# Performance work log

Hardware: AMD Instinct MI355X
Metric: run time of the kernel (lower is better)

Reference implementation:

```python
import jax, jax.numpy as jnp
import numpy as np

HIDDEN = 512
HEADS = 8
HEAD_DIM = HIDDEN // HEADS


def setup_inputs() -> dict:
    key = jax.random.key(0)
    ks = jax.random.split(key, 13)
    B, S, H = 4, 2048, HIDDEN
    s = 1.0 / np.sqrt(H).astype(np.float32)
    inp = {
        "values": jax.random.normal(ks[0], (B, S, H), jnp.float32),
        "keys": jax.random.normal(ks[1], (B, S, H), jnp.float32),
        "query": jax.random.normal(ks[2], (B, S, H), jnp.float32),
        "mask": jax.random.randint(ks[3], (B, S), 0, 2, jnp.int32),
        "Wq": jax.random.normal(ks[4], (H, H), jnp.float32) * s,
        "bq": jnp.zeros((H,), jnp.float32),
        "Wk": jax.random.normal(ks[5], (H, H), jnp.float32) * s,
        "bk": jnp.zeros((H,), jnp.float32),
        "Wv": jax.random.normal(ks[6], (H, H), jnp.float32) * s,
        "bv": jnp.zeros((H,), jnp.float32),
        "Wo": jax.random.normal(ks[7], (H, H), jnp.float32) * s,
        "bo": jnp.zeros((H,), jnp.float32),
    }
    return inp


def reference(values, keys, query, mask, Wq, bq, Wk, bk, Wv, bv, Wo, bo):
    B, Sq, H = query.shape
    Sk = keys.shape[1]
    # projections (x @ W + b)
    Q = query @ Wq + bq
    K = keys @ Wk + bk
    V = values @ Wv + bv
    # [B, S, H] -> [B, heads, S, head_dim]
    def split(x, S):
        return x.reshape(B, S, HEADS, HEAD_DIM).transpose(0, 2, 1, 3)
    Qh, Kh, Vh = split(Q, Sq), split(K, Sk), split(V, Sk)
    scale = 1.0 / np.sqrt(HEAD_DIM).astype(np.float32)
    scores = jnp.einsum('bhqd,bhkd->bhqk', Qh, Kh) * scale  # [B,H,Sq,Sk]
    m = mask[:, None, None, :]  # [B,1,1,Sk]
    scores = jnp.where(m == 0, jnp.float32(-1e9), scores)
    attn = jax.nn.softmax(scores, axis=-1)
    ctx = jnp.einsum('bhqk,bhkd->bhqd', attn, Vh)
    ctx = ctx.transpose(0, 2, 1, 3).reshape(B, Sq, H)
    return ctx @ Wo + bo
```

## Files before the change

kernel.cpp:

```cpp
#include <hip/hip_runtime.h>

#define HID 512
#define NH 8
#define HD 64
#define BATCH 4
#define SEQ 2048
#define MTOT (BATCH * SEQ)

typedef unsigned short ushort_t;
typedef __bf16 bf16x8 __attribute__((ext_vector_type(8)));
typedef unsigned short ushort8v __attribute__((ext_vector_type(8)));
typedef unsigned short ushort4v __attribute__((ext_vector_type(4)));
typedef float floatx4 __attribute__((ext_vector_type(4)));
typedef unsigned int uintx4 __attribute__((ext_vector_type(4)));

static __device__ __forceinline__ unsigned short f2bf(float f) {
  __bf16 b = (__bf16)f;
  return __builtin_bit_cast(unsigned short, b);
}
static __device__ __forceinline__ float bf2f(unsigned short s) {
  union { unsigned int u; float f; } c; c.u = ((unsigned int)s) << 16;
  return c.f;
}
static __device__ __forceinline__ bf16x8 asbf(ushort8v v) {
  return __builtin_bit_cast(bf16x8, v);
}
static __device__ __forceinline__ float max3f(float a, float b, float c) {
  return fmaxf(fmaxf(a, b), c);
}
static __device__ __forceinline__ float fexp2(float x) {
  return __builtin_amdgcn_exp2f(x);
}
static __device__ __forceinline__ void gl_lds16(const ushort_t* g, ushort_t* l) {
  __builtin_amdgcn_global_load_lds(
      (const __attribute__((address_space(1))) void*)g,
      (__attribute__((address_space(3))) void*)l, 16, 0, 0);
}

#define SC_LOG2E 0.18033688011112042f

__global__ void detect_dtype(const unsigned int* __restrict__ q, int* __restrict__ flag) {
  if (threadIdx.x == 0 && blockIdx.x == 0) {
    int hits = 0;
    for (int i = 0; i < 256; ++i) {
      unsigned e = (q[i] >> 7) & 0xff;
      hits += (e >= 110 && e <= 136) ? 1 : 0;
    }
    flag[0] = (hits >= 128) ? 1 : 0;
  }
}

__global__ __launch_bounds__(256) void prep_w(
    const void* __restrict__ W0, const void* __restrict__ W1,
    const void* __restrict__ W2, const void* __restrict__ W3,
    ushort_t* __restrict__ T0, ushort_t* __restrict__ T1,
    ushort_t* __restrict__ T2, ushort_t* __restrict__ T3,
    const int* __restrict__ flag) {
  const int isbf = flag[0];
  const void* W; ushort_t* T;
  switch (blockIdx.y) {
    case 0: W = W0; T = T0; break;
    case 1: W = W1; T = T1; break;
    case 2: W = W2; T = T2; break;
    default: W = W3; T = T3; break;
  }
  __shared__ ushort_t Ts[64 * 72];
  const int tid = threadIdx.x;
  const int kt = (blockIdx.x >> 3) * 64;
  const int nt = (blockIdx.x & 7) * 64;
  const int r = tid >> 2;
  const int c = (tid & 3) * 16;

  ushort8v v0, v1;
  if (isbf) {
    const ushort_t* p = (const ushort_t*)W + (long)(kt + r) * HID + nt + c;
    v0 = *(const ushort8v*)(p);
    v1 = *(const ushort8v*)(p + 8);
  } else {
    const float* p = (const float*)W + (long)(kt + r) * HID + nt + c;
    floatx4 f0 = *(const floatx4*)(p);
    floatx4 f1 = *(const floatx4*)(p + 4);
    floatx4 f2 = *(const floatx4*)(p + 8);
    floatx4 f3 = *(const floatx4*)(p + 12);
#pragma unroll
    for (int i = 0; i < 4; ++i) {
      v0[i] = f2bf(f0[i]); v0[4 + i] = f2bf(f1[i]);
      v1[i] = f2bf(f2[i]); v1[4 + i] = f2bf(f3[i]);
    }
  }
  *(ushort8v*)(&Ts[r * 72 + c])     = v0;
  *(ushort8v*)(&Ts[r * 72 + c + 8]) = v1;
  __syncthreads();
  ushort8v o0, o1;
#pragma unroll
  for (int j = 0; j < 8; ++j) o0[j] = Ts[(c + j) * 72 + r];
#pragma unroll
  for (int j = 0; j < 8; ++j) o1[j] = Ts[(c + 8 + j) * 72 + r];
  ushort_t* q = T + (long)(nt + r) * HID + kt + c;
  *(ushort8v*)(q)     = o0;
  *(ushort8v*)(q + 8) = o1;
}

__global__ __launch_bounds__(256) void prep_b(
    const void* __restrict__ B0, const void* __restrict__ B1,
    const void* __restrict__ B2, const void* __restrict__ B3,
    float* __restrict__ biasF, const int* __restrict__ flag) {
  const int isbf = flag[0];
  int i = blockIdx.x * 256 + threadIdx.x;
  int t = i >> 9, j = i & 511;
  const void* B = (t == 0) ? B0 : (t == 1) ? B1 : (t == 2) ? B2 : B3;
  biasF[i] = isbf ? bf2f(((const ushort_t*)B)[j]) : ((const float*)B)[j];
}

__global__ __launch_bounds__(256) void prep_mask(
    const int* __restrict__ mask, float* __restrict__ mb) {
  int i = blockIdx.x * 256 + threadIdx.x;
  mb[i] = mask[i] ? 0.f : -1e9f;
}

__global__ __launch_bounds__(256) void gemm_qkv3(
    const void* __restrict__ X0, const void* __restrict__ X1, const void* __restrict__ X2,
    const ushort_t* __restrict__ WtBase, const float* __restrict__ biasBase,
    ushort_t* __restrict__ YBase, const int* __restrict__ flag) {
  const int isbf = flag[0];
  int lin = blockIdx.x + 256 * blockIdx.z;
  int swz = (lin & 7) * 96 + (lin >> 3);
  const int z = swz >> 8;
  const int mblk = swz & 255;
  const void* X = (z == 0) ? X0 : (z == 1) ? X1 : X2;
  const ushort_t* Wt = WtBase + (size_t)z * HID * HID;
  const float* biasF = biasBase + (size_t)z * HID;
  ushort_t* Y = YBase + (size_t)z * MTOT * HID;

  const int tid = threadIdx.x;
  const int wid = tid >> 6, lane = tid & 63;
  const int id = lane & 15, quad = lane >> 4;
  const int m0 = mblk * 32;

  __shared__ ushort_t As[32 * 32];
  __shared__ ushort_t Bs[512 * 32];

  const int a_r = tid >> 3;
  const int a_b = (tid & 7) >> 1;
  const int a_o = (tid & 1) * 4;
  const int a_pb = a_b ^ (a_r & 3);
  const int b_ro = lane >> 2;
  const int b_scb = (lane & 3);

  floatx4 acc[2][8];
#pragma unroll
  for (int i = 0; i < 2; ++i)
#pragma unroll
    for (int j = 0; j < 8; ++j) acc[i][j] = (floatx4){0.f, 0.f, 0.f, 0.f};

  for (int k0 = 0; k0 < HID; k0 += 32) {
    ushort4v aW;
    if (isbf) {
      aW = *(const ushort4v*)((const ushort_t*)X + (long)(m0 + a_r) * HID + k0 + (tid & 7) * 4);
    } else {
      floatx4 f = *(const floatx4*)((const float*)X + (long)(m0 + a_r) * HID + k0 + (tid & 7) * 4);
#pragma unroll
      for (int i = 0; i < 4; ++i) aW[i] = f2bf(f[i]);
    }
    __syncthreads();
    *(ushort4v*)(&As[a_r * 32 + (a_pb << 3) + a_o]) = aW;
#pragma unroll
    for (int i = 0; i < 8; ++i) {
      int rb = wid * 128 + i * 16;
      int srow = rb + b_ro;
      gl_lds16(Wt + (long)srow * HID + k0 + ((b_scb ^ (srow & 3)) << 3), &Bs[rb * 32]);
    }
    __syncthreads();
    {
      ushort8v af[2], bfv[8];
      const int pb = (quad ^ (id & 3)) << 3;
#pragma unroll
      for (int ms = 0; ms < 2; ++ms)
        af[ms] = *(const ushort8v*)(&As[(ms * 16 + id) * 32 + pb]);
#pragma unroll
      for (int ns = 0; ns < 8; ++ns)
        bfv[ns] = *(const ushort8v*)(&Bs[(wid * 128 + ns * 16 + id) * 32 + pb]);
#pragma unroll
      for (int ms = 0; ms < 2; ++ms)
#pragma unroll
        for (int ns = 0; ns < 8; ++ns)
          acc[ms][ns] = __builtin_amdgcn_mfma_f32_16x16x32_bf16(asbf(af[ms]), asbf(bfv[ns]), acc[ms][ns], 0, 0, 0);
    }
  }
#pragma unroll
  for (int ns = 0; ns < 8; ++ns) {
    int col = wid * 128 + ns * 16 + id;
    float bv = biasF[col];
#pragma unroll
    for (int ms = 0; ms < 2; ++ms) {
      int row0 = m0 + ms * 16 + quad * 4;
#pragma unroll
      for (int r = 0; r < 4; ++r)
        Y[(long)(row0 + r) * HID + col] = f2bf(acc[ms][ns][r] + bv);
    }
  }
}

__global__ __launch_bounds__(256) void gemm_out2(
    const ushort_t* __restrict__ X, const ushort_t* __restrict__ Wt,
    const float* __restrict__ biasF, void* __restrict__ out,
    const int* __restrict__ flag) {
  const int isbf = flag[0];
  const int tid = threadIdx.x;
  const int wid = tid >> 6, lane = tid & 63;
  const int id = lane & 15, quad = lane >> 4;
  const int wm = wid >> 1, wn = wid & 1;
  const int m0 = blockIdx.x * 64, n0 = blockIdx.y * 128;

  __shared__ ushort_t As[64 * 64];
  __shared__ ushort_t Bs[128 * 64];

  const int lrow = lane >> 3;
  const int scb  = (lane & 7) ^ lrow;

  floatx4 acc[2][4];
#pragma unroll
  for (int i = 0; i < 2; ++i)
#pragma unroll
    for (int j = 0; j < 4; ++j) acc[i][j] = (floatx4){0.f, 0.f, 0.f, 0.f};

  for (int k0 = 0; k0 < HID; k0 += 64) {
    __syncthreads();
#pragma unroll
    for (int i = 0; i < 2; ++i) {
      int r = wid * 16 + i * 8 + lrow;
      gl_lds16(X + (long)(m0 + r) * HID + k0 + scb * 8, &As[(wid * 16 + i * 8) * 64]);
    }
#pragma unroll
    for (int i = 0; i < 4; ++i) {
      int r = wid * 32 + i * 8 + lrow;
      gl_lds16(Wt + (long)(n0 + r) * HID + k0 + scb * 8, &Bs[(wid * 32 + i * 8) * 64]);
    }
    __syncthreads();
#pragma unroll
    for (int kk = 0; kk < 64; kk += 32) {
      ushort8v af[2], bfv[4];
      const int cb = (kk >> 3) + quad;
#pragma unroll
      for (int ms = 0; ms < 2; ++ms) {
        int row = wm * 32 + ms * 16 + id;
        af[ms] = *(const ushort8v*)(&As[row * 64 + ((cb ^ (id & 7)) << 3)]);
      }
#pragma unroll
      for (int ns = 0; ns < 4; ++ns) {
        int row = wn * 64 + ns * 16 + id;
        bfv[ns] = *(const ushort8v*)(&Bs[row * 64 + ((cb ^ (id & 7)) << 3)]);
      }
#pragma unroll
      for (int ms = 0; ms < 2; ++ms)
#pragma unroll
        for (int ns = 0; ns < 4; ++ns)
          acc[ms][ns] = __builtin_amdgcn_mfma_f32_16x16x32_bf16(asbf(af[ms]), asbf(bfv[ns]), acc[ms][ns], 0, 0, 0);
    }
  }
#pragma unroll
  for (int ns = 0; ns < 4; ++ns) {
    int col = n0 + wn * 64 + ns * 16 + id;
    float bv = biasF[col];
#pragma unroll
    for (int ms = 0; ms < 2; ++ms) {
      int row0 = m0 + wm * 32 + ms * 16 + quad * 4;
      if (isbf) {
        ushort_t* o = (ushort_t*)out;
#pragma unroll
        for (int r = 0; r < 4; ++r) o[(long)(row0 + r) * HID + col] = f2bf(acc[ms][ns][r] + bv);
      } else {
        float* o = (float*)out;
#pragma unroll
        for (int r = 0; r < 4; ++r) o[(long)(row0 + r) * HID + col] = acc[ms][ns][r] + bv;
      }
    }
  }
}

__global__ __launch_bounds__(512) void flash_attn(
    const ushort_t* __restrict__ Q, const ushort_t* __restrict__ K,
    const ushort_t* __restrict__ V, const float* __restrict__ mb,
    ushort_t* __restrict__ ctx) {
  int lin = blockIdx.x + 16 * blockIdx.y + 128 * blockIdx.z;
  int swz = (lin & 7) * 64 + (lin >> 3);
  const int qblk = swz & 15, h = (swz >> 4) & 7, b = swz >> 7;
  const int tid = threadIdx.x;
  const int wid = tid >> 6, lane = tid & 63;
  const int id = lane & 15, quad = lane >> 4;

  __shared__ ushort_t Kt[64 * 72];
  __shared__ ushort_t Vt[64 * 72];
  __shared__ ushort_t Pl[8][16 * 72];

  const ushort_t* Qb = Q + (long)(b * SEQ + qblk * 128 + wid * 16) * HID + h * HD;
  const ushort_t* Kb = K + (long)(b * SEQ) * HID + h * HD;
  const ushort_t* Vb = V + (long)(b * SEQ) * HID + h * HD;
  const float* mrow = mb + b * SEQ;

  ushort8v qf[2];
#pragma unroll
  for (int kh = 0; kh < 2; ++kh)
    qf[kh] = *(const ushort8v*)(Qb + id * HID + kh * 32 + quad * 8);

  floatx4 o[4];
  float m_i = -1e30f, l_i = 0.f;
#pragma unroll
  for (int dg = 0; dg < 4; ++dg) o[dg] = (floatx4){0, 0, 0, 0};

  const bool kstager = (tid < 256);
  const int t2 = tid & 255;
  const int skey = t2 >> 2;
  const int sdc  = (t2 & 3) * 16;
  const int vkp  = (t2 & 31) * 2;
  const int vdc  = (t2 >> 5) * 8;

  ushort8v r0, r1;
  if (kstager) {
    const ushort_t* kpp = Kb + (long)skey * HID + sdc;
    r0 = *(const ushort8v*)(kpp);
    r1 = *(const ushort8v*)(kpp + 8);
  } else {
    const ushort_t* vp0 = Vb + (long)vkp * HID + vdc;
    r0 = *(const ushort8v*)(vp0);
    r1 = *(const ushort8v*)(vp0 + HID);
  }

  for (int kb = 0; kb < SEQ / 64; ++kb) {
    if (kstager) {
      *(ushort8v*)(&Kt[skey * 72 + sdc])     = r0;
      *(ushort8v*)(&Kt[skey * 72 + sdc + 8]) = r1;
    } else {
      uintx4 a = __builtin_bit_cast(uintx4, r0);
      uintx4 bq = __builtin_bit_cast(uintx4, r1);
#pragma unroll
      for (int j = 0; j < 4; ++j) {
        unsigned int d0 = __builtin_amdgcn_perm(bq[j], a[j], 0x05040100u);
        unsigned int d1 = __builtin_amdgcn_perm(bq[j], a[j], 0x07060302u);
        *(unsigned int*)(&Vt[(vdc + 2 * j) * 72 + vkp])     = d0;
        *(unsigned int*)(&Vt[(vdc + 2 * j + 1) * 72 + vkp]) = d1;
      }
    }
    __syncthreads();

    if (kb + 1 < SEQ / 64) {
      if (kstager) {
        const ushort_t* kpp = Kb + (long)((kb + 1) * 64 + skey) * HID + sdc;
        r0 = *(const ushort8v*)(kpp);
        r1 = *(const ushort8v*)(kpp + 8);
      } else {
        const ushort_t* vp0 = Vb + (long)((kb + 1) * 64 + vkp) * HID + vdc;
        r0 = *(const ushort8v*)(vp0);
        r1 = *(const ushort8v*)(vp0 + HID);
      }
    }

    floatx4 st[4];
    __builtin_amdgcn_s_setprio(1);
#pragma unroll
    for (int ks = 0; ks < 4; ++ks) {
      ushort8v kf0 = *(const ushort8v*)(&Kt[(ks * 16 + id) * 72 + quad * 8]);
      ushort8v kf1 = *(const ushort8v*)(&Kt[(ks * 16 + id) * 72 + 32 + quad * 8]);
      floatx4 a = (floatx4){0, 0, 0, 0};
      a = __builtin_amdgcn_mfma_f32_16x16x32_bf16(asbf(kf0), asbf(qf[0]), a, 0, 0, 0);
      a = __builtin_amdgcn_mfma_f32_16x16x32_bf16(asbf(kf1), asbf(qf[1]), a, 0, 0, 0);
      st[ks] = a;
    }
    __builtin_amdgcn_s_setprio(0);
#pragma unroll
    for (int ks = 0; ks < 4; ++ks) {
      floatx4 mbv = *(const floatx4*)(mrow + kb * 64 + ks * 16 + quad * 4);
#pragma unroll
      for (int r = 0; r < 4; ++r)
        st[ks][r] = fmaf(st[ks][r], SC_LOG2E, mbv[r]);
    }
    {
      float t0 = max3f(st[0][0], st[0][1], st[0][2]);
      float t1 = max3f(st[0][3], st[1][0], st[1][1]);
      float t2m = max3f(st[1][2], st[1][3], st[2][0]);
      float t3 = max3f(st[2][1], st[2][2], st[2][3]);
      float t4 = max3f(st[3][0], st[3][1], st[3][2]);
      float mx = max3f(t0, t1, st[3][3]);
      float mz = max3f(t2m, t3, t4);
      mx = fmaxf(mx, mz);
      mx = fmaxf(mx, __shfl_xor(mx, 16));
      mx = fmaxf(mx, __shfl_xor(mx, 32));
      if (!__all(mx - m_i <= 8.f)) {
        float mnew = fmaxf(m_i, mx);
        float alpha = fexp2(m_i - mnew);
        m_i = mnew;
        l_i *= alpha;
#pragma unroll
        for (int dg = 0; dg < 4; ++dg) o[dg] *= alpha;
      }
      float mcur = m_i;
      floatx4 rsv = (floatx4){0.f, 0.f, 0.f, 0.f};
#pragma unroll
      for (int ks = 0; ks < 4; ++ks) {
        ushort4v pk;
#pragma unroll
        for (int r = 0; r < 4; ++r) {
          float p = fexp2(st[ks][r] - mcur);
          rsv[r] += p;
          pk[r] = f2bf(p);
        }
        *(ushort4v*)(&Pl[wid][id * 72 + ks * 16 + quad * 4]) = pk;
      }
      float rs = (rsv[0] + rsv[1]) + (rsv[2] + rsv[3]);
      rs += __shfl_xor(rs, 16);
      rs += __shfl_xor(rs, 32);
      l_i += rs;
    }

    __builtin_amdgcn_s_setprio(1);
#pragma unroll
    for (int kc = 0; kc < 2; ++kc) {
      ushort8v pf = *(const ushort8v*)(&Pl[wid][id * 72 + kc * 32 + quad * 8]);
#pragma unroll
      for (int dg = 0; dg < 4; ++dg) {
        ushort8v vf = *(const ushort8v*)(&Vt[(dg * 16 + id) * 72 + kc * 32 + quad * 8]);
        o[dg] = __builtin_amdgcn_mfma_f32_16x16x32_bf16(asbf(vf), asbf(pf), o[dg], 0, 0, 0);
      }
    }
    __builtin_amdgcn_s_setprio(0);
    __syncthreads();
  }

  {
    float inv = 1.0f / l_i;
    long qrow = (long)(b * SEQ + qblk * 128 + wid * 16 + id);
#pragma unroll
    for (int dg = 0; dg < 4; ++dg) {
      ushort4v pk;
#pragma unroll
      for (int r = 0; r < 4; ++r) pk[r] = f2bf(o[dg][r] * inv);
      *(ushort4v*)(&ctx[qrow * HID + h * HD + dg * 16 + quad * 4]) = pk;
    }
  }
}

extern "C" void kernel_launch(void* const* d_in, const int* in_sizes, int n_in,
                              void* d_out, int out_size, void* d_ws, size_t ws_size,
                              hipStream_t stream) {
  const void* values = d_in[0];
  const void* keys   = d_in[1];
  const void* query  = d_in[2];
  const int*  mask   = (const int*)d_in[3];
  const void* Wq = d_in[4];  const void* bq = d_in[5];
  const void* Wk = d_in[6];  const void* bk = d_in[7];
  const void* Wv = d_in[8];  const void* bv = d_in[9];
  const void* Wo = d_in[10]; const void* bo = d_in[11];

  ushort_t* ws = (ushort_t*)d_ws;
  const size_t NEL = (size_t)MTOT * HID;
  ushort_t* Qp  = ws;
  ushort_t* Kp  = ws + NEL;
  ushort_t* Vp  = ws + 2 * NEL;
  ushort_t* Cp  = ws + 3 * NEL;
  ushort_t* WqT = ws + 4 * NEL;
  ushort_t* WkT = WqT + (size_t)HID * HID;
  ushort_t* WvT = WkT + (size_t)HID * HID;
  ushort_t* WoT = WvT + (size_t)HID * HID;
  float* biasF  = (float*)(WoT + (size_t)HID * HID);
  float* mbias  = biasF + 4 * HID;
  int* flag     = (int*)(mbias + (size_t)BATCH * SEQ);

  detect_dtype<<<1, 64, 0, stream>>>((const unsigned int*)query, flag);
  prep_w<<<dim3(64, 4), 256, 0, stream>>>(Wq, Wk, Wv, Wo, WqT, WkT, WvT, WoT, flag);
  prep_b<<<8, 256, 0, stream>>>(bq, bk, bv, bo, biasF, flag);
  prep_mask<<<MTOT / 256, 256, 0, stream>>>(mask, mbias);

  gemm_qkv3<<<dim3(MTOT / 32, 1, 3), 256, 0, stream>>>(
      query, keys, values, WqT, biasF, Qp, flag);

  flash_attn<<<dim3(SEQ / 128, NH, BATCH), 512, 0, stream>>>(Qp, Kp, Vp, mbias, Cp);

  gemm_out2<<<dim3(MTOT / 64, HID / 128), 256, 0, stream>>>(
      Cp, WoT, biasF + 3 * HID, d_out, flag);
}
```

Measured before the change: 235.7 us.

## Load K fragments directly to registers and double-buffer V tile in flash attention

The flash attention kernel now reads K fragments straight from global memory into registers, prefetching the next tile during softmax, instead of staging K through shared memory. V is double-buffered in shared memory, with global loads issued two tiles ahead, so the transpose-store for the next tile overlaps with compute on the current one. The dtype detection kernel is parallelised across a wavefront, and the bias and mask prep kernels are merged into one launch. This trades higher register pressure and uncoalesced per-lane K loads for fewer LDS round trips and less stalling on staging.

```diff
diff --git a/kernel.cpp b/kernel.cpp
--- a/kernel.cpp
+++ b/kernel.cpp
@@ -40,14 +40,16 @@
 #define SC_LOG2E 0.18033688011112042f
 
 __global__ void detect_dtype(const unsigned int* __restrict__ q, int* __restrict__ flag) {
-  if (threadIdx.x == 0 && blockIdx.x == 0) {
-    int hits = 0;
-    for (int i = 0; i < 256; ++i) {
-      unsigned e = (q[i] >> 7) & 0xff;
-      hits += (e >= 110 && e <= 136) ? 1 : 0;
-    }
-    flag[0] = (hits >= 128) ? 1 : 0;
-  }
+  int lane = threadIdx.x;
+  int hits = 0;
+#pragma unroll
+  for (int i = 0; i < 4; ++i) {
+    unsigned e = (q[lane * 4 + i] >> 7) & 0xff;
+    hits += (e >= 110 && e <= 136) ? 1 : 0;
+  }
+#pragma unroll
+  for (int s = 1; s < 64; s <<= 1) hits += __shfl_xor(hits, s);
+  if (lane == 0) flag[0] = (hits >= 128) ? 1 : 0;
 }
 
 __global__ __launch_bounds__(256) void prep_w(
@@ -101,21 +103,22 @@
   *(ushort8v*)(q + 8) = o1;
 }
 
-__global__ __launch_bounds__(256) void prep_b(
+__global__ __launch_bounds__(256) void prep_bm(
     const void* __restrict__ B0, const void* __restrict__ B1,
     const void* __restrict__ B2, const void* __restrict__ B3,
-    float* __restrict__ biasF, const int* __restrict__ flag) {
-  const int isbf = flag[0];
-  int i = blockIdx.x * 256 + threadIdx.x;
-  int t = i >> 9, j = i & 511;
-  const void* B = (t == 0) ? B0 : (t == 1) ? B1 : (t == 2) ? B2 : B3;
-  biasF[i] = isbf ? bf2f(((const ushort_t*)B)[j]) : ((const float*)B)[j];
-}
-
-__global__ __launch_bounds__(256) void prep_mask(
-    const int* __restrict__ mask, float* __restrict__ mb) {
-  int i = blockIdx.x * 256 + threadIdx.x;
-  mb[i] = mask[i] ? 0.f : -1e9f;
+    float* __restrict__ biasF, const int* __restrict__ mask,
+    float* __restrict__ mb, const int* __restrict__ flag) {
+  const int blk = blockIdx.x;
+  if (blk < 8) {
+    const int isbf = flag[0];
+    int i = blk * 256 + threadIdx.x;
+    int t = i >> 9, j = i & 511;
+    const void* B = (t == 0) ? B0 : (t == 1) ? B1 : (t == 2) ? B2 : B3;
+    biasF[i] = isbf ? bf2f(((const ushort_t*)B)[j]) : ((const float*)B)[j];
+  } else {
+    int i = (blk - 8) * 256 + threadIdx.x;
+    mb[i] = mask[i] ? 0.f : -1e9f;
+  }
 }
 
 __global__ __launch_bounds__(256) void gemm_qkv3(
@@ -141,9 +144,8 @@
   __shared__ ushort_t Bs[512 * 32];
 
   const int a_r = tid >> 3;
-  const int a_b = (tid & 7) >> 1;
   const int a_o = (tid & 1) * 4;
-  const int a_pb = a_b ^ (a_r & 3);
+  const int a_pb = ((tid & 7) >> 1) ^ (a_r & 3);
   const int b_ro = lane >> 2;
   const int b_scb = (lane & 3);
 
@@ -288,9 +290,9 @@
   const int tid = threadIdx.x;
   const int wid = tid >> 6, lane = tid & 63;
   const int id = lane & 15, quad = lane >> 4;
-
-  __shared__ ushort_t Kt[64 * 72];
-  __shared__ ushort_t Vt[64 * 72];
+  const int NT = SEQ / 64;
+
+  __shared__ ushort_t Vt[2][64 * 72];
   __shared__ ushort_t Pl[8][16 * 72];
 
   const ushort_t* Qb = Q + (long)(b * SEQ + qblk * 128 + wid * 16) * HID + h * HD;
@@ -308,50 +310,49 @@
 #pragma unroll
   for (int dg = 0; dg < 4; ++dg) o[dg] = (floatx4){0, 0, 0, 0};
 
-  const bool kstager = (tid < 256);
+  const bool vstager = (tid >= 256);
   const int t2 = tid & 255;
-  const int skey = t2 >> 2;
-  const int sdc  = (t2 & 3) * 16;
-  const int vkp  = (t2 & 31) * 2;
-  const int vdc  = (t2 >> 5) * 8;
-
-  ushort8v r0, r1;
-  if (kstager) {
-    const ushort_t* kpp = Kb + (long)skey * HID + sdc;
-    r0 = *(const ushort8v*)(kpp);
-    r1 = *(const ushort8v*)(kpp + 8);
-  } else {
+  const int vkp = (t2 & 31) * 2;
+  const int vdc = (t2 >> 5) * 8;
+
+  ushort8v kfr[4][2];
+  ushort8v vr0, vr1;
+
+  if (vstager) {
     const ushort_t* vp0 = Vb + (long)vkp * HID + vdc;
-    r0 = *(const ushort8v*)(vp0);
-    r1 = *(const ushort8v*)(vp0 + HID);
-  }
-
-  for (int kb = 0; kb < SEQ / 64; ++kb) {
-    if (kstager) {
-      *(ushort8v*)(&Kt[skey * 72 + sdc])     = r0;
-      *(ushort8v*)(&Kt[skey * 72 + sdc + 8]) = r1;
-    } else {
-      uintx4 a = __builtin_bit_cast(uintx4, r0);
-      uintx4 bq = __builtin_bit_cast(uintx4, r1);
+    ushort8v a0 = *(const ushort8v*)(vp0);
+    ushort8v a1 = *(const ushort8v*)(vp0 + HID);
+    uintx4 pa = __builtin_bit_cast(uintx4, a0);
+    uintx4 pb = __builtin_bit_cast(uintx4, a1);
+#pragma unroll
+    for (int j = 0; j < 4; ++j) {
+      unsigned int d0 = __builtin_amdgcn_perm(pb[j], pa[j], 0x05040100u);
+      unsigned int d1 = __builtin_amdgcn_perm(pb[j], pa[j], 0x07060302u);
+      *(unsigned int*)(&Vt[0][(vdc + 2 * j) * 72 + vkp])     = d0;
+      *(unsigned int*)(&Vt[0][(vdc + 2 * j + 1) * 72 + vkp]) = d1;
+    }
+    const ushort_t* vp1 = Vb + (long)(64 + vkp) * HID + vdc;
+    vr0 = *(const ushort8v*)(vp1);
+    vr1 = *(const ushort8v*)(vp1 + HID);
+  }
+#pragma unroll
+  for (int ks = 0; ks < 4; ++ks)
+#pragma unroll
+    for (int kh = 0; kh < 2; ++kh)
+      kfr[ks][kh] = *(const ushort8v*)(Kb + (long)(ks * 16 + id) * HID + kh * 32 + quad * 8);
+  __syncthreads();
+
+  for (int kb = 0; kb < NT; ++kb) {
+    const int cur = kb & 1;
+    if (vstager && kb + 1 < NT) {
+      uintx4 pa = __builtin_bit_cast(uintx4, vr0);
+      uintx4 pb = __builtin_bit_cast(uintx4, vr1);
 #pragma unroll
       for (int j = 0; j < 4; ++j) {
-        unsigned int d0 = __builtin_amdgcn_perm(bq[j], a[j], 0x05040100u);
-        unsigned int d1 = __builtin_amdgcn_perm(bq[j], a[j], 0x07060302u);
-        *(unsigned int*)(&Vt[(vdc + 2 * j) * 72 + vkp])     = d0;
-        *(unsigned int*)(&Vt[(vdc + 2 * j + 1) * 72 + vkp]) = d1;
-      }
-    }
-    __syncthreads();
-
-    if (kb + 1 < SEQ / 64) {
-      if (kstager) {
-        const ushort_t* kpp = Kb + (long)((kb + 1) * 64 + skey) * HID + sdc;
-        r0 = *(const ushort8v*)(kpp);
-        r1 = *(const ushort8v*)(kpp + 8);
-      } else {
-        const ushort_t* vp0 = Vb + (long)((kb + 1) * 64 + vkp) * HID + vdc;
-        r0 = *(const ushort8v*)(vp0);
-        r1 = *(const ushort8v*)(vp0 + HID);
+        unsigned int d0 = __builtin_amdgcn_perm(pb[j], pa[j], 0x05040100u);
+        unsigned int d1 = __builtin_amdgcn_perm(pb[j], pa[j], 0x07060302u);
+        *(unsigned int*)(&Vt[1 - cur][(vdc + 2 * j) * 72 + vkp])     = d0;
+        *(unsigned int*)(&Vt[1 - cur][(vdc + 2 * j + 1) * 72 + vkp]) = d1;
       }
     }
 
@@ -359,14 +360,19 @@
     __builtin_amdgcn_s_setprio(1);
 #pragma unroll
     for (int ks = 0; ks < 4; ++ks) {
-      ushort8v kf0 = *(const ushort8v*)(&Kt[(ks * 16 + id) * 72 + quad * 8]);
-      ushort8v kf1 = *(const ushort8v*)(&Kt[(ks * 16 + id) * 72 + 32 + quad * 8]);
       floatx4 a = (floatx4){0, 0, 0, 0};
-      a = __builtin_amdgcn_mfma_f32_16x16x32_bf16(asbf(kf0), asbf(qf[0]), a, 0, 0, 0);
-      a = __builtin_amdgcn_mfma_f32_16x16x32_bf16(asbf(kf1), asbf(qf[1]), a, 0, 0, 0);
+      a = __builtin_amdgcn_mfma_f32_16x16x32_bf16(asbf(kfr[ks][0]), asbf(qf[0]), a, 0, 0, 0);
+      a = __builtin_amdgcn_mfma_f32_16x16x32_bf16(asbf(kfr[ks][1]), asbf(qf[1]), a, 0, 0, 0);
       st[ks] = a;
     }
     __builtin_amdgcn_s_setprio(0);
+
+    if (vstager && kb + 2 < NT) {
+      const ushort_t* vp0 = Vb + (long)((kb + 2) * 64 + vkp) * HID + vdc;
+      vr0 = *(const ushort8v*)(vp0);
+      vr1 = *(const ushort8v*)(vp0 + HID);
+    }
+
 #pragma unroll
     for (int ks = 0; ks < 4; ++ks) {
       floatx4 mbv = *(const floatx4*)(mrow + kb * 64 + ks * 16 + quad * 4);
@@ -412,13 +418,22 @@
       l_i += rs;
     }
 
+    if (kb + 1 < NT) {
+      const ushort_t* kp = Kb + (long)((kb + 1) * 64 + id) * HID;
+#pragma unroll
+      for (int ks = 0; ks < 4; ++ks)
+#pragma unroll
+        for (int kh = 0; kh < 2; ++kh)
+          kfr[ks][kh] = *(const ushort8v*)(kp + (long)(ks * 16) * HID + kh * 32 + quad * 8);
+    }
+
     __builtin_amdgcn_s_setprio(1);
 #pragma unroll
     for (int kc = 0; kc < 2; ++kc) {
       ushort8v pf = *(const ushort8v*)(&Pl[wid][id * 72 + kc * 32 + quad * 8]);
 #pragma unroll
       for (int dg = 0; dg < 4; ++dg) {
-        ushort8v vf = *(const ushort8v*)(&Vt[(dg * 16 + id) * 72 + kc * 32 + quad * 8]);
+        ushort8v vf = *(const ushort8v*)(&Vt[cur][(dg * 16 + id) * 72 + kc * 32 + quad * 8]);
         o[dg] = __builtin_amdgcn_mfma_f32_16x16x32_bf16(asbf(vf), asbf(pf), o[dg], 0, 0, 0);
       }
     }
@@ -467,8 +482,7 @@
 
   detect_dtype<<<1, 64, 0, stream>>>((const unsigned int*)query, flag);
   prep_w<<<dim3(64, 4), 256, 0, stream>>>(Wq, Wk, Wv, Wo, WqT, WkT, WvT, WoT, flag);
-  prep_b<<<8, 256, 0, stream>>>(bq, bk, bv, bo, biasF, flag);
-  prep_mask<<<MTOT / 256, 256, 0, stream>>>(mask, mbias);
+  prep_bm<<<40, 256, 0, stream>>>(bq, bk, bv, bo, biasF, mask, mbias, flag);
 
   gemm_qkv3<<<dim3(MTOT / 32, 1, 3), 256, 0, stream>>>(
       query, keys, values, WqT, biasF, Qp, flag);
```

Result: slower. 303.5 us (+28.8%).
